# Kernel optimization log

Measured on AMD Instinct MI355X. Metric: run time of the kernel, lower is better.

Reference implementation:

```python
import jax, jax.numpy as jnp
import numpy as np


def setup_inputs() -> dict:
    key = jax.random.key(0)
    k1, k2 = jax.random.split(key)
    B, N, M, K = 8, 4096, 4096, 64
    input1 = jax.random.normal(k1, (B, N, K), dtype=jnp.float32)
    input2 = jax.random.normal(k2, (B, M, K), dtype=jnp.float32)
    return {"input1": input1, "input2": input2}


def reference(input1, input2):
    # Pairwise L2 distances via the ||x||^2 + ||y||^2 - 2<x,y> identity,
    # avoiding the O(B*N*M*K) broadcast-subtraction intermediate.
    x2 = jnp.sum(input1 * input1, axis=-1)                 # [B, N]
    y2 = jnp.sum(input2 * input2, axis=-1)                 # [B, M]
    xy = jnp.einsum('bnk,bmk->bnm', input1, input2)        # [B, N, M]
    sq = x2[:, :, None] + y2[:, None, :] - 2.0 * xy
    D = jnp.sqrt(jnp.maximum(sq, 0.0))                     # [B, N, M]
    dist0 = jnp.mean(jnp.min(D, axis=1), axis=1)           # min over N, mean over M
    dist1 = jnp.mean(jnp.min(D, axis=2), axis=1)           # min over M, mean over N
    loss = jnp.mean(dist0 + dist1)
    return loss
```

## Files before the change

### kernel.cpp

```cpp
#include <hip/hip_runtime.h>

#define BATCH 8
#define NPTS  4096
#define KD    64
#define MQ    4
#define WALK  8
#define FINF  3.0e38f

typedef float f32x4 __attribute__((ext_vector_type(4)));
typedef float f32x2 __attribute__((ext_vector_type(2)));
typedef short s16x8 __attribute__((ext_vector_type(8)));

__device__ __forceinline__ unsigned int f2bf(float f) {
  unsigned int u = __float_as_uint(f);
  u += 0x7FFFu + ((u >> 16) & 1u);
  return u >> 16;
}

__device__ __forceinline__ void stage16(const void* g, void* l) {
  __builtin_amdgcn_global_load_lds((const __attribute__((address_space(1))) void*)g,
                                   (__attribute__((address_space(3))) void*)l, 16, 0, 0);
}

__global__ __launch_bounds__(256)
void prep_kernel(const float* __restrict__ X, const float* __restrict__ Y,
                 unsigned int* __restrict__ Xbf, unsigned int* __restrict__ Ybf,
                 float* __restrict__ x2, float* __restrict__ y2,
                 unsigned int* __restrict__ minbuf,
                 unsigned int* __restrict__ counter) {
  int gid = blockIdx.x * 256 + threadIdx.x;
  if (gid == 0) *counter = 0;
  if (gid < 2 * BATCH * NPTS) minbuf[gid] = 0x7F800000u;
  int row = gid >> 5;
  int ki  = gid & 31;
  bool isX = row < BATCH * NPTS;
  int r2 = row & (BATCH * NPTS - 1);
  const float* src = isX ? X : Y;
  f32x2 v = *(const f32x2*)(src + (size_t)r2 * KD + ki * 2);
  float s = v[0] * v[0] + v[1] * v[1];
  #pragma unroll
  for (int m = 16; m >= 1; m >>= 1) s += __shfl_xor(s, m, 64);
  unsigned int packed = (f2bf(v[1]) << 16) | f2bf(v[0]);
  (isX ? Xbf : Ybf)[r2 * 32 + ki] = packed;
  if (ki == 0) (isX ? x2 : y2)[r2] = s;
}

__global__ __launch_bounds__(256, 2)
void chamfer_main(const unsigned short* __restrict__ Xbf,
                  const unsigned short* __restrict__ Ybf,
                  const float* __restrict__ x2g, const float* __restrict__ y2g,
                  unsigned int* __restrict__ rowmin,
                  unsigned int* __restrict__ colmin) {
  __shared__ __align__(16) unsigned short Ys[2][128 * 64];
  __shared__ float l_credq[2 * 4 * 132];
  __shared__ float l_redf[256];

  const int lin = blockIdx.x;
  const int logical = (lin & 7) * 128 + (lin >> 3);
  const int mq = logical & 3, ntile = (logical >> 2) & 31, b = logical >> 7;
  const int n0 = ntile * 128;
  const int mbase = mq * (WALK * 128);
  const int t = threadIdx.x, w = t >> 6, lane = t & 63, c = lane & 15, q = lane >> 4;
  const int wr = (w >> 1) * 64, wc = (w & 1) * 64, rg = w >> 1;

  const int l8 = lane >> 3;
  const int lane_off = l8 * 128 + (((lane & 7) ^ l8) << 4);

  const unsigned short* Xrow = Xbf + (size_t)(b * NPTS + n0) * KD;
  const char* Yg0 = (const char*)(Ybf + (size_t)(b * NPTS + mbase) * KD);

  #pragma unroll
  for (int k = 0; k < 4; ++k)
    stage16(Yg0 + (k * 32 + w * 8) * 128 + lane_off,
            (char*)Ys[0] + (k * 256 + w * 64) * 16);

  s16x8 xf[4][2];
  #pragma unroll
  for (int i = 0; i < 4; ++i)
    #pragma unroll
    for (int ks = 0; ks < 2; ++ks)
      xf[i][ks] = *(const s16x8*)&Xrow[(size_t)(wr + i * 16 + c) * KD + (ks * 4 + q) * 8];

  const float* x2b = x2g + b * NPTS + n0;
  f32x4 x2r[4];
  #pragma unroll
  for (int i = 0; i < 4; ++i) x2r[i] = *(const f32x4*)(x2b + wr + i * 16 + q * 4);

  __syncthreads();

  float rm[4][4];
  #pragma unroll
  for (int i = 0; i < 4; ++i)
    #pragma unroll
    for (int r = 0; r < 4; ++r) rm[i][r] = FINF;

  const int cx = c & 7;
  const float* y2b = y2g + b * NPTS + mbase;
  unsigned int* colbase = colmin + (size_t)b * NPTS + mbase;
  const f32x4 zacc = {0.f, 0.f, 0.f, 0.f};

  #pragma unroll 2
  for (int tt = 0; tt < WALK; ++tt) {
    const unsigned short* cur = Ys[tt & 1];

    float y2c[4];
    #pragma unroll
    for (int j = 0; j < 4; ++j) y2c[j] = y2b[tt * 128 + wc + j * 16 + c];

    if (tt < WALK - 1) {
      const char* Ygt = Yg0 + (size_t)(tt + 1) * 128 * 128;
      unsigned short* nb = Ys[(tt + 1) & 1];
      #pragma unroll
      for (int k = 0; k < 4; ++k)
        stage16(Ygt + (k * 32 + w * 8) * 128 + lane_off,
                (char*)nb + (k * 256 + w * 64) * 16);
    }

    if (tt > 0 && t < 128) {
      int pt = tt - 1, pb = pt & 1;
      float v = fminf(fminf(l_credq[(pb * 4 + 0) * 132 + t], l_credq[(pb * 4 + 1) * 132 + t]),
                      fminf(l_credq[(pb * 4 + 2) * 132 + t], l_credq[(pb * 4 + 3) * 132 + t]));
      float d = fmaxf(v + y2b[pt * 128 + t], 0.f);
      atomicMin(&colbase[pt * 128 + t], __float_as_uint(d));
    }

    float cmj[4];
    #pragma unroll
    for (int j = 0; j < 4; ++j) {
      const unsigned short* yrow = &cur[(wc + j * 16 + c) * 64];
      s16x8 yf0 = *(const s16x8*)&yrow[(q ^ cx) << 3];
      s16x8 yf1 = *(const s16x8*)&yrow[((4 + q) ^ cx) << 3];
      f32x4 acc[4];
      #pragma unroll
      for (int i = 0; i < 4; ++i) {
        f32x4 a0 = __builtin_amdgcn_mfma_f32_16x16x32_bf16(xf[i][0], yf0, zacc, 0, 0, 0);
        acc[i] = __builtin_amdgcn_mfma_f32_16x16x32_bf16(xf[i][1], yf1, a0, 0, 0, 0);
      }
      float cm = FINF;
      #pragma unroll
      for (int i = 0; i < 4; ++i)
        #pragma unroll
        for (int r = 0; r < 4; ++r) {
          float v = acc[i][r];
          rm[i][r] = fminf(rm[i][r], fmaf(-2.f, v, y2c[j]));
          cm = fminf(cm, fmaf(-2.f, v, x2r[i][r]));
        }
      cm = fminf(cm, __shfl_xor(cm, 16, 64));
      cmj[j] = cm;
    }
    {
      int s = rg * 2 + (q >> 1);
      int jA = (q & 1) * 2;
      float sA = (q & 1) ? cmj[2] : cmj[0];
      float sB = (q & 1) ? cmj[3] : cmj[1];
      float* dst = &l_credq[((tt & 1) * 4 + s) * 132 + wc + c];
      dst[jA * 16]      = sA;
      dst[jA * 16 + 16] = sB;
    }

    __syncthreads();
  }

  #pragma unroll
  for (int msk = 1; msk <= 8; msk <<= 1)
    #pragma unroll
    for (int i = 0; i < 4; ++i)
      #pragma unroll
      for (int r = 0; r < 4; ++r)
        rm[i][r] = fminf(rm[i][r], __shfl_xor(rm[i][r], msk, 64));
  if (c == 0) {
    #pragma unroll
    for (int i = 0; i < 4; ++i) {
      f32x4 v = {rm[i][0], rm[i][1], rm[i][2], rm[i][3]};
      *(f32x4*)&l_redf[w * 64 + i * 16 + q * 4] = v;
    }
  }
  __syncthreads();

  if (t < 128) {
    {
      int pt = WALK - 1, pb = pt & 1;
      float v = fminf(fminf(l_credq[(pb * 4 + 0) * 132 + t], l_credq[(pb * 4 + 1) * 132 + t]),
                      fminf(l_credq[(pb * 4 + 2) * 132 + t], l_credq[(pb * 4 + 3) * 132 + t]));
      float d = fmaxf(v + y2b[pt * 128 + t], 0.f);
      atomicMin(&colbase[pt * 128 + t], __float_as_uint(d));
    }
    int g = t >> 6, lr = t & 63;
    float v = fminf(l_redf[(g * 2) * 64 + lr], l_redf[(g * 2 + 1) * 64 + lr]) + x2b[t];
    atomicMin(&rowmin[(size_t)b * NPTS + n0 + t], __float_as_uint(fmaxf(v, 0.f)));
  }
}

__global__ __launch_bounds__(256)
void reduce_kernel(const unsigned int* __restrict__ rowmin,
                   const unsigned int* __restrict__ colmin,
                   float* __restrict__ partials, unsigned int* __restrict__ counter,
                   float* __restrict__ out) {
  int i = blockIdx.x * 256 + threadIdx.x;
  const int TOT = BATCH * NPTS;
  float s0 = sqrtf(__uint_as_float(rowmin[i])) + sqrtf(__uint_as_float(colmin[i]));
  #pragma unroll
  for (int m = 32; m >= 1; m >>= 1) s0 += __shfl_xor(s0, m, 64);
  __shared__ float wsum[4];
  if ((threadIdx.x & 63) == 0) wsum[threadIdx.x >> 6] = s0;
  __syncthreads();

  if (threadIdx.x < 64) {
    unsigned int ticket = 0;
    if (threadIdx.x == 0) {
      float bsum = wsum[0] + wsum[1] + wsum[2] + wsum[3];
      atomicExch(&partials[blockIdx.x], bsum);
      __threadfence();
      ticket = atomicAdd(counter, 1);
    }
    ticket = __shfl(ticket, 0, 64);
    if (ticket == 127) {
      float v = atomicAdd(&partials[threadIdx.x], 0.0f) +
                atomicAdd(&partials[threadIdx.x + 64], 0.0f);
      #pragma unroll
      for (int m = 32; m >= 1; m >>= 1) v += __shfl_xor(v, m, 64);
      if (threadIdx.x == 0) out[0] = v * (1.0f / (float)TOT);
    }
  }
}

extern "C" void kernel_launch(void* const* d_in, const int* in_sizes, int n_in,
                              void* d_out, int out_size, void* d_ws, size_t ws_size,
                              hipStream_t stream) {
  const float* X = (const float*)d_in[0];
  const float* Y = (const float*)d_in[1];
  float* out = (float*)d_out;

  char* ws = (char*)d_ws;
  unsigned int* Xbf = (unsigned int*)ws;
  unsigned int* Ybf = (unsigned int*)(ws + (4u << 20));
  float* x2 = (float*)(ws + (8u << 20));
  float* y2 = (float*)(ws + (8u << 20) + (128u << 10));
  unsigned int* minbuf = (unsigned int*)(ws + (8u << 20) + (256u << 10));
  unsigned int* rowmin = minbuf;
  unsigned int* colmin = minbuf + BATCH * NPTS;
  float* partials = (float*)(ws + (8u << 20) + (512u << 10));
  unsigned int* counter = (unsigned int*)(partials + 128);

  prep_kernel<<<dim3(2 * BATCH * NPTS * 32 / 256), dim3(256), 0, stream>>>(
      X, Y, Xbf, Ybf, x2, y2, minbuf, counter);

  chamfer_main<<<dim3(MQ * 32 * BATCH), dim3(256), 0, stream>>>(
      (const unsigned short*)Xbf, (const unsigned short*)Ybf, x2, y2, rowmin, colmin);

  reduce_kernel<<<dim3(BATCH * NPTS / 256), dim3(256), 0, stream>>>(
      rowmin, colmin, partials, counter, out);
}
```

Measured before the change: 105.1 us.

## Fuse final reduction into main kernel via last-block ticket and use v_min3

Removes the separate reduce kernel launch. The last chamfer_main block, found through an atomic ticket counter, now sums sqrt of all row and column minima, which it reads with atomic loads. The column-min accumulation is also rewritten as a tree of v_min3_f32 instructions instead of a serial fminf chain. The tail reduction now runs in one block, walking 64K elements serially with atomics, in exchange for dropping a launch.

```diff
diff --git a/kernel.cpp b/kernel.cpp
--- a/kernel.cpp
+++ b/kernel.cpp
@@ -20,6 +20,12 @@
 __device__ __forceinline__ void stage16(const void* g, void* l) {
   __builtin_amdgcn_global_load_lds((const __attribute__((address_space(1))) void*)g,
                                    (__attribute__((address_space(3))) void*)l, 16, 0, 0);
+}
+
+__device__ __forceinline__ float min3f(float a, float b, float c) {
+  float d;
+  asm("v_min3_f32 %0, %1, %2, %3" : "=v"(d) : "v"(a), "v"(b), "v"(c));
+  return d;
 }
 
 __global__ __launch_bounds__(256)
@@ -50,10 +56,13 @@
                   const unsigned short* __restrict__ Ybf,
                   const float* __restrict__ x2g, const float* __restrict__ y2g,
                   unsigned int* __restrict__ rowmin,
-                  unsigned int* __restrict__ colmin) {
+                  unsigned int* __restrict__ colmin,
+                  unsigned int* __restrict__ counter,
+                  float* __restrict__ out) {
   __shared__ __align__(16) unsigned short Ys[2][128 * 64];
   __shared__ float l_credq[2 * 4 * 132];
   __shared__ float l_redf[256];
+  __shared__ unsigned int s_ticket;
 
   const int lin = blockIdx.x;
   const int logical = (lin & 7) * 128 + (lin >> 3);
@@ -136,15 +145,22 @@
         f32x4 a0 = __builtin_amdgcn_mfma_f32_16x16x32_bf16(xf[i][0], yf0, zacc, 0, 0, 0);
         acc[i] = __builtin_amdgcn_mfma_f32_16x16x32_bf16(xf[i][1], yf1, a0, 0, 0, 0);
       }
-      float cm = FINF;
+      float u[16];
       #pragma unroll
       for (int i = 0; i < 4; ++i)
         #pragma unroll
         for (int r = 0; r < 4; ++r) {
           float v = acc[i][r];
           rm[i][r] = fminf(rm[i][r], fmaf(-2.f, v, y2c[j]));
-          cm = fminf(cm, fmaf(-2.f, v, x2r[i][r]));
+          u[i * 4 + r] = fmaf(-2.f, v, x2r[i][r]);
         }
+      float c0 = min3f(u[0],  u[1],  u[2]);
+      float c1 = min3f(u[3],  u[4],  u[5]);
+      float c2 = min3f(u[6],  u[7],  u[8]);
+      float c3 = min3f(u[9],  u[10], u[11]);
+      float c4 = min3f(u[12], u[13], u[14]);
+      float c5 = min3f(c0, c1, u[15]);
+      float cm = fminf(min3f(c2, c3, c4), c5);
       cm = fminf(cm, __shfl_xor(cm, 16, 64));
       cmj[j] = cm;
     }
@@ -189,38 +205,27 @@
     float v = fminf(l_redf[(g * 2) * 64 + lr], l_redf[(g * 2 + 1) * 64 + lr]) + x2b[t];
     atomicMin(&rowmin[(size_t)b * NPTS + n0 + t], __float_as_uint(fmaxf(v, 0.f)));
   }
-}
-
-__global__ __launch_bounds__(256)
-void reduce_kernel(const unsigned int* __restrict__ rowmin,
-                   const unsigned int* __restrict__ colmin,
-                   float* __restrict__ partials, unsigned int* __restrict__ counter,
-                   float* __restrict__ out) {
-  int i = blockIdx.x * 256 + threadIdx.x;
-  const int TOT = BATCH * NPTS;
-  float s0 = sqrtf(__uint_as_float(rowmin[i])) + sqrtf(__uint_as_float(colmin[i]));
-  #pragma unroll
-  for (int m = 32; m >= 1; m >>= 1) s0 += __shfl_xor(s0, m, 64);
-  __shared__ float wsum[4];
-  if ((threadIdx.x & 63) == 0) wsum[threadIdx.x >> 6] = s0;
-  __syncthreads();
-
-  if (threadIdx.x < 64) {
-    unsigned int ticket = 0;
-    if (threadIdx.x == 0) {
-      float bsum = wsum[0] + wsum[1] + wsum[2] + wsum[3];
-      atomicExch(&partials[blockIdx.x], bsum);
-      __threadfence();
-      ticket = atomicAdd(counter, 1);
-    }
-    ticket = __shfl(ticket, 0, 64);
-    if (ticket == 127) {
-      float v = atomicAdd(&partials[threadIdx.x], 0.0f) +
-                atomicAdd(&partials[threadIdx.x + 64], 0.0f);
-      #pragma unroll
-      for (int m = 32; m >= 1; m >>= 1) v += __shfl_xor(v, m, 64);
-      if (threadIdx.x == 0) out[0] = v * (1.0f / (float)TOT);
-    }
+
+  __syncthreads();
+  if (t == 0) {
+    __threadfence();
+    s_ticket = atomicAdd(counter, 1);
+  }
+  __syncthreads();
+  if (s_ticket == MQ * 32 * BATCH - 1) {
+    const int TOT = BATCH * NPTS;
+    float s0 = 0.f;
+    for (int i = t; i < TOT; i += 256) {
+      unsigned int rv = atomicMin(&rowmin[i], 0xFFFFFFFFu);
+      unsigned int cv = atomicMin(&colmin[i], 0xFFFFFFFFu);
+      s0 += sqrtf(__uint_as_float(rv)) + sqrtf(__uint_as_float(cv));
+    }
+    #pragma unroll
+    for (int m = 32; m >= 1; m >>= 1) s0 += __shfl_xor(s0, m, 64);
+    if (lane == 0) l_redf[w] = s0;
+    __syncthreads();
+    if (t == 0)
+      out[0] = (l_redf[0] + l_redf[1] + l_redf[2] + l_redf[3]) * (1.0f / (float)TOT);
   }
 }
 
@@ -239,15 +244,12 @@
   unsigned int* minbuf = (unsigned int*)(ws + (8u << 20) + (256u << 10));
   unsigned int* rowmin = minbuf;
   unsigned int* colmin = minbuf + BATCH * NPTS;
-  float* partials = (float*)(ws + (8u << 20) + (512u << 10));
-  unsigned int* counter = (unsigned int*)(partials + 128);
+  unsigned int* counter = (unsigned int*)(ws + (8u << 20) + (512u << 10));
 
   prep_kernel<<<dim3(2 * BATCH * NPTS * 32 / 256), dim3(256), 0, stream>>>(
       X, Y, Xbf, Ybf, x2, y2, minbuf, counter);
 
   chamfer_main<<<dim3(MQ * 32 * BATCH), dim3(256), 0, stream>>>(
-      (const unsigned short*)Xbf, (const unsigned short*)Ybf, x2, y2, rowmin, colmin);
-
-  reduce_kernel<<<dim3(BATCH * NPTS / 256), dim3(256), 0, stream>>>(
-      rowmin, colmin, partials, counter, out);
-}
+      (const unsigned short*)Xbf, (const unsigned short*)Ybf, x2, y2,
+      rowmin, colmin, counter, out);
+}
```

After: 155.2 us. 47.7% more time.
